# Kernel tuning notes

Measured on AMD Instinct MI355X. Metric: run time of the kernel, lower is better.

Reference implementation:

```python
import jax, jax.numpy as jnp
import numpy as np
from jax import lax

# dims
BS, C, H, W = 16, 684, 32, 128   # batch, encoder channels, feature-map H/W
Q, K, PAD = 256, 11, 5           # coverage channels, conv_Q kernel, padding
N, NP = 256, 512                 # decoder hidden n, attention dim n_prime
T = 4                            # prior attention steps stored in alpha


def setup_inputs() -> dict:
    key = jax.random.key(0)
    ks = jax.random.split(key, 10)
    s = 0.02  # small init scale (stand-in for xavier)
    return {
        "x": jax.random.normal(ks[0], (BS, C, H, W), jnp.float32),
        "st_hat": jax.random.normal(ks[1], (BS, 1, N), jnp.float32),
        "alpha": jax.random.uniform(ks[2], (BS, T, H * W), jnp.float32),
        # conv_Q: Conv2d(1, Q, k=11, pad=5)
        "convQ_w": jax.random.normal(ks[3], (Q, 1, K, K), jnp.float32) * s,
        "convQ_b": jnp.zeros((Q,), jnp.float32),
        # fc_Wa: Linear(n, n_prime)
        "Wa_w": jax.random.normal(ks[4], (NP, N), jnp.float32) * s,
        "Wa_b": jnp.zeros((NP,), jnp.float32),
        # conv_Ua: Conv2d(C, n_prime, k=1)
        "convUa_w": jax.random.normal(ks[5], (NP, C, 1, 1), jnp.float32) * s,
        "convUa_b": jnp.zeros((NP,), jnp.float32),
        # fc_Uf: Linear(Q, n_prime)
        "Uf_w": jax.random.normal(ks[6], (NP, Q), jnp.float32) * s,
        "Uf_b": jnp.zeros((NP,), jnp.float32),
        # fc_Va: Linear(n_prime, 1)
        "Va_w": jax.random.normal(ks[7], (1, NP), jnp.float32) * s,
        "Va_b": jnp.zeros((1,), jnp.float32),
    }


def reference(x, st_hat, alpha, convQ_w, convQ_b, Wa_w, Wa_b,
              convUa_w, convUa_b, Uf_w, Uf_b, Va_w, Va_b):
    bs, c, h, w = x.shape
    # beta: sum of past attention maps -> [bs, 1, h, w]
    beta = alpha.sum(axis=1).reshape(bs, 1, h, w)
    # conv_Q: coverage features [bs, Q, h, w]
    Fc = lax.conv_general_dilated(
        beta, convQ_w, window_strides=(1, 1), padding=[(PAD, PAD), (PAD, PAD)],
        dimension_numbers=("NCHW", "OIHW", "NCHW")) + convQ_b[None, :, None, None]
    # fc_Uf over channel dim after permute(2,3,0,1): [h, w, bs, n_prime]
    cover = jnp.einsum("bqhw,pq->hwbp", Fc, Uf_w) + Uf_b
    # conv_Ua (1x1 conv == per-pixel linear): [h, w, bs, n_prime]
    key = jnp.einsum("bchw,pc->hwbp", x, convUa_w[:, :, 0, 0]) + convUa_b
    # fc_Wa(st_hat).squeeze(1): [bs, n_prime]
    query = st_hat[:, 0, :] @ Wa_w.T + Wa_b
    # additive attention score
    score = jnp.tanh(key + query[None, None, :, :] + cover)  # [h,w,bs,np]
    # fc_Va -> e_t, permuted to [bs, h*w] (row-major over h,w like torch view)
    e = jnp.einsum("hwbp,p->bhw", score, Va_w[0]) + Va_b[0]
    e = e.reshape(bs, h * w)
    # softmax with the module's explicit exp/sum + eps formulation
    e_exp = jnp.exp(e)
    alpha_t = e_exp / (e_exp.sum(axis=1, keepdims=True) + 1e-8)  # [bs, hw]
    # context vector g_t = sum_n alpha_t[b,n] * x[b,c,n]
    context = jnp.einsum("bn,bcn->bc", alpha_t, x.reshape(bs, c, h * w))
    return context, alpha_t.reshape(bs, 1, h, w)
```

## Files before the change

### kernel.cpp

```cpp
#include <hip/hip_runtime.h>
#include <math.h>

#define BS 16
#define C_ 684
#define Hh 32
#define Ww 128
#define HW 4096
#define Qc 256
#define NP 512
#define Nn 256
#define NKT 26
#define NB 64

#define WS_BETA 0
#define WS_BIAS 65536
#define WS_EEXP 73728
#define WS_ESUM 139264
#define WS_ASW  139280

typedef __attribute__((ext_vector_type(8))) short bf16x8;
typedef __attribute__((ext_vector_type(4))) float f32x4;

static __device__ __forceinline__ short f2bf(float f) {
    unsigned u = __builtin_bit_cast(unsigned, f);
    u += 0x7fff + ((u >> 16) & 1);
    return (short)(u >> 16);
}

static __device__ __forceinline__ float fast_tanh(float v) {
    float ax = fabsf(v);
    float t = __expf(-2.f * ax);
    float th = (1.f - t) * __builtin_amdgcn_rcpf(1.f + t);
    return copysignf(th, v);
}

__global__ void k_prep(const float* __restrict__ alpha, const float* __restrict__ ua,
                       const float* __restrict__ ufw, const float* __restrict__ qw,
                       const float* __restrict__ st, const float* __restrict__ waw,
                       const float* __restrict__ wab, const float* __restrict__ ufb,
                       const float* __restrict__ qb, const float* __restrict__ uab,
                       float* __restrict__ beta, short* __restrict__ a_sw,
                       float* __restrict__ bias, float* __restrict__ esum) {
    int part = blockIdx.x, tid = threadIdx.x;
    if (part < 256) {
        int idx = part * 256 + tid;
        int b = idx >> 12, n = idx & 4095;
        const float* a = alpha + (size_t)b * 4 * HW + n;
        beta[idx] = a[0] + a[HW] + a[2 * HW] + a[3 * HW];
    } else if (part < 1920) {
        int idx = (part - 256) * 256 + tid;
        int j = idx & 7, m = (idx >> 3) & 511, g = (idx >> 12) & 3, kt = idx >> 14;
        int k = kt * 32 + g * 8 + j;
        float v = 0.f;
        if (k < C_) {
            v = ua[m * C_ + k];
        } else if (k < C_ + 121) {
            int tap = k - C_;
            const float* ur = ufw + m * Qc;
            float s = 0.f;
            for (int q = 0; q < Qc; ++q) s += ur[q] * qw[q * 121 + tap];
            v = s;
        }
        a_sw[idx] = f2bf(v);
    } else if (part < 1952) {
        int idx = (part - 1920) * 256 + tid;
        int b = idx >> 9, p = idx & 511;
        float s = wab[p] + ufb[p] + uab[p];
        const float* sv = st + b * Nn;
        const float* wr = waw + p * Nn;
        for (int n = 0; n < Nn; ++n) s += sv[n] * wr[n];
        const float* ur = ufw + p * Qc;
        for (int q = 0; q < Qc; ++q) s += ur[q] * qb[q];
        bias[idx] = s;
    } else {
        if (tid < BS) esum[tid] = 0.f;
    }
}

__launch_bounds__(256, 2)
__global__ void k_gemm(const short* __restrict__ a_sw, const float* __restrict__ x,
                       const float* __restrict__ beta, const float* __restrict__ bias,
                       const float* __restrict__ vaw, const float* __restrict__ vab,
                       float* __restrict__ eexp, float* __restrict__ esum) {
    __shared__ short Bs[2][4 * NB * 8];
    __shared__ float ered[4][NB];

    const int tid = threadIdx.x;
    const int lane = tid & 63, wid = tid >> 6;
    const int b = blockIdx.y, n0 = blockIdx.x * NB;
    const int q = lane >> 4, r = lane & 15;

    const int sn = tid & 63;
    const int sg = tid >> 6;
    const int n_glob = n0 + sn;
    const int pr = n_glob >> 7, pc = n_glob & 127;
    const float* xb = x + (size_t)b * C_ * HW + n_glob;
    const float* betab = beta + b * HW;

    f32x4 acc[8][4] = {};
    float fv[2][8];

    #define LDSTAGE(KT, DST)                                                  \
    {                                                                         \
        int kbase = (KT) * 32 + sg * 8;                                       \
        _Pragma("unroll")                                                     \
        for (int j = 0; j < 8; ++j) {                                         \
            int k = kbase + j;                                                \
            float f = 0.f;                                                    \
            if (k < C_) {                                                     \
                f = xb[(size_t)k * HW];                                       \
            } else if (k < C_ + 121) {                                        \
                int tap = k - C_;                                             \
                int di = tap / 11, dj = tap - di * 11;                        \
                int rr = pr + di - 5, cc = pc + dj - 5;                       \
                if (rr >= 0 && rr < Hh && cc >= 0 && cc < Ww)                 \
                    f = betab[rr * 128 + cc];                                 \
            }                                                                 \
            (DST)[j] = f;                                                     \
        }                                                                     \
    }

    LDSTAGE(0, fv[0]);
    LDSTAGE(1, fv[1]);

    const short* ap = a_sw + (size_t)(q * NP + wid * 128 + r) * 8;

    #pragma unroll 2
    for (int kt = 0; kt < NKT; ++kt) {
        bf16x8 af[8];
        const short* ak = ap + (size_t)kt * 4 * NP * 8;
        #pragma unroll
        for (int ms = 0; ms < 8; ++ms)
            af[ms] = *(const bf16x8*)(ak + ms * 16 * 8);

        {
            const float* f = fv[kt & 1];
            unsigned pk[4];
            #pragma unroll
            for (int h = 0; h < 4; ++h)
                pk[h] = (unsigned)(unsigned short)f2bf(f[2 * h]) |
                        ((unsigned)(unsigned short)f2bf(f[2 * h + 1]) << 16);
            *(uint4*)&Bs[kt & 1][(sg * NB + sn) * 8] = make_uint4(pk[0], pk[1], pk[2], pk[3]);
        }
        __syncthreads();

        bf16x8 bf[4];
        #pragma unroll
        for (int ns = 0; ns < 4; ++ns)
            bf[ns] = *(const bf16x8*)&Bs[kt & 1][(q * NB + ns * 16 + r) * 8];

        if (kt < NKT - 2) LDSTAGE(kt + 2, fv[kt & 1]);

        #pragma unroll
        for (int ms = 0; ms < 8; ++ms)
            #pragma unroll
            for (int ns = 0; ns < 4; ++ns)
                acc[ms][ns] = __builtin_amdgcn_mfma_f32_16x16x32_bf16(af[ms], bf[ns], acc[ms][ns], 0, 0, 0);
    }
    #undef LDSTAGE

    float es[4] = {0.f, 0.f, 0.f, 0.f};
    #pragma unroll
    for (int ms = 0; ms < 8; ++ms) {
        #pragma unroll
        for (int reg = 0; reg < 4; ++reg) {
            int row = wid * 128 + ms * 16 + q * 4 + reg;
            float bv = bias[b * NP + row];
            float vv = vaw[row];
            #pragma unroll
            for (int ns = 0; ns < 4; ++ns)
                es[ns] += vv * fast_tanh(acc[ms][ns][reg] + bv);
        }
    }
    #pragma unroll
    for (int ns = 0; ns < 4; ++ns) {
        es[ns] += __shfl_xor(es[ns], 16, 64);
        es[ns] += __shfl_xor(es[ns], 32, 64);
    }
    if (lane < 16) {
        #pragma unroll
        for (int ns = 0; ns < 4; ++ns) ered[wid][ns * 16 + r] = es[ns];
    }
    __syncthreads();
    if (tid < NB) {
        float s = ered[0][tid] + ered[1][tid] + ered[2][tid] + ered[3][tid] + vab[0];
        float ex = expf(s);
        eexp[b * HW + n0 + tid] = ex;
        float ps = ex;
        #pragma unroll
        for (int off = 32; off > 0; off >>= 1) ps += __shfl_xor(ps, off, 64);
        if (tid == 0) atomicAdd(&esum[b], ps);
    }
}

__global__ void k_finish(const float* __restrict__ x, const float* __restrict__ eexp,
                         const float* __restrict__ esum, float* __restrict__ ctx,
                         float* __restrict__ aout) {
    int part = blockIdx.x, b = blockIdx.y, tid = threadIdx.x;
    float iv = 1.f / (esum[b] + 1e-8f);
    if (part == 171) {
        for (int k = tid; k < HW; k += 256) aout[b * HW + k] = eexp[b * HW + k] * iv;
        return;
    }
    int wid = tid >> 6, lane = tid & 63;
    int c = part * 4 + wid;
    const float4* xr = (const float4*)(x + ((size_t)b * C_ + c) * HW);
    const float4* er = (const float4*)(eexp + b * HW);
    float acc = 0.f;
    #pragma unroll 8
    for (int k = lane; k < 1024; k += 64) {
        float4 xv = xr[k], ev = er[k];
        acc += xv.x * ev.x + xv.y * ev.y + xv.z * ev.z + xv.w * ev.w;
    }
    #pragma unroll
    for (int off = 32; off > 0; off >>= 1) acc += __shfl_xor(acc, off, 64);
    if (lane == 0) ctx[b * C_ + c] = acc * iv;
}

extern "C" void kernel_launch(void* const* d_in, const int* in_sizes, int n_in,
                              void* d_out, int out_size, void* d_ws, size_t ws_size,
                              hipStream_t stream) {
    const float* x      = (const float*)d_in[0];
    const float* st     = (const float*)d_in[1];
    const float* alpha  = (const float*)d_in[2];
    const float* convQw = (const float*)d_in[3];
    const float* convQb = (const float*)d_in[4];
    const float* Waw    = (const float*)d_in[5];
    const float* Wab    = (const float*)d_in[6];
    const float* Uaw    = (const float*)d_in[7];
    const float* Uab    = (const float*)d_in[8];
    const float* Ufw    = (const float*)d_in[9];
    const float* Ufb    = (const float*)d_in[10];
    const float* Vaw    = (const float*)d_in[11];
    const float* Vab    = (const float*)d_in[12];

    float* ws   = (float*)d_ws;
    float* beta = ws + WS_BETA;
    float* bias = ws + WS_BIAS;
    float* eexp = ws + WS_EEXP;
    float* esum = ws + WS_ESUM;
    short* a_sw = (short*)(ws + WS_ASW);

    float* ctx  = (float*)d_out;
    float* aout = (float*)d_out + BS * C_;

    k_prep<<<1953, 256, 0, stream>>>(alpha, Uaw, Ufw, convQw, st, Waw, Wab, Ufb,
                                     convQb, Uab, beta, a_sw, bias, esum);
    k_gemm<<<dim3(HW / NB, BS), 256, 0, stream>>>(a_sw, x, beta, bias, Vaw, Vab, eexp, esum);
    k_finish<<<dim3(172, BS), 256, 0, stream>>>(x, eexp, esum, ctx, aout);
}
```

Baseline: 366.8 us.

## Split attention GEMM across M halves with atomic score accumulation and separate softmax pass

Splits the 512-row attention dimension across two blocks per pixel tile, halving accumulators and raising the occupancy target. Partial scores are accumulated by atomics into a zeroed buffer. A new small kernel then computes exp and the per-batch normalizer. Each half re-streams the x/beta operand, doubling global reads and bf16 conversion work, and the change adds one launch.

```diff
diff --git a/kernel.cpp b/kernel.cpp
--- a/kernel.cpp
+++ b/kernel.cpp
@@ -15,8 +15,9 @@
 #define WS_BETA 0
 #define WS_BIAS 65536
 #define WS_EEXP 73728
-#define WS_ESUM 139264
-#define WS_ASW  139280
+#define WS_E    139264
+#define WS_INV  204800
+#define WS_ASW  204816
 
 typedef __attribute__((ext_vector_type(8))) short bf16x8;
 typedef __attribute__((ext_vector_type(4))) float f32x4;
@@ -40,7 +41,7 @@
                        const float* __restrict__ wab, const float* __restrict__ ufb,
                        const float* __restrict__ qb, const float* __restrict__ uab,
                        float* __restrict__ beta, short* __restrict__ a_sw,
-                       float* __restrict__ bias, float* __restrict__ esum) {
+                       float* __restrict__ bias, float* __restrict__ e) {
     int part = blockIdx.x, tid = threadIdx.x;
     if (part < 256) {
         int idx = part * 256 + tid;
@@ -73,22 +74,23 @@
         for (int q = 0; q < Qc; ++q) s += ur[q] * qb[q];
         bias[idx] = s;
     } else {
-        if (tid < BS) esum[tid] = 0.f;
-    }
-}
-
-__launch_bounds__(256, 2)
+        e[(part - 1952) * 256 + tid] = 0.f;
+    }
+}
+
+__launch_bounds__(256, 3)
 __global__ void k_gemm(const short* __restrict__ a_sw, const float* __restrict__ x,
                        const float* __restrict__ beta, const float* __restrict__ bias,
                        const float* __restrict__ vaw, const float* __restrict__ vab,
-                       float* __restrict__ eexp, float* __restrict__ esum) {
+                       float* __restrict__ e) {
     __shared__ short Bs[2][4 * NB * 8];
     __shared__ float ered[4][NB];
 
     const int tid = threadIdx.x;
     const int lane = tid & 63, wid = tid >> 6;
-    const int b = blockIdx.y, n0 = blockIdx.x * NB;
+    const int b = blockIdx.z, my = blockIdx.y, n0 = blockIdx.x * NB;
     const int q = lane >> 4, r = lane & 15;
+    const int m0 = my * 256;
 
     const int sn = tid & 63;
     const int sg = tid >> 6;
@@ -97,7 +99,7 @@
     const float* xb = x + (size_t)b * C_ * HW + n_glob;
     const float* betab = beta + b * HW;
 
-    f32x4 acc[8][4] = {};
+    f32x4 acc[4][4] = {};
     float fv[2][8];
 
     #define LDSTAGE(KT, DST)                                                  \
@@ -123,14 +125,14 @@
     LDSTAGE(0, fv[0]);
     LDSTAGE(1, fv[1]);
 
-    const short* ap = a_sw + (size_t)(q * NP + wid * 128 + r) * 8;
+    const short* ap = a_sw + (size_t)(q * NP + m0 + wid * 64 + r) * 8;
 
     #pragma unroll 2
     for (int kt = 0; kt < NKT; ++kt) {
-        bf16x8 af[8];
+        bf16x8 af[4];
         const short* ak = ap + (size_t)kt * 4 * NP * 8;
         #pragma unroll
-        for (int ms = 0; ms < 8; ++ms)
+        for (int ms = 0; ms < 4; ++ms)
             af[ms] = *(const bf16x8*)(ak + ms * 16 * 8);
 
         {
@@ -152,7 +154,7 @@
         if (kt < NKT - 2) LDSTAGE(kt + 2, fv[kt & 1]);
 
         #pragma unroll
-        for (int ms = 0; ms < 8; ++ms)
+        for (int ms = 0; ms < 4; ++ms)
             #pragma unroll
             for (int ns = 0; ns < 4; ++ns)
                 acc[ms][ns] = __builtin_amdgcn_mfma_f32_16x16x32_bf16(af[ms], bf[ns], acc[ms][ns], 0, 0, 0);
@@ -161,10 +163,10 @@
 
     float es[4] = {0.f, 0.f, 0.f, 0.f};
     #pragma unroll
-    for (int ms = 0; ms < 8; ++ms) {
+    for (int ms = 0; ms < 4; ++ms) {
         #pragma unroll
         for (int reg = 0; reg < 4; ++reg) {
-            int row = wid * 128 + ms * 16 + q * 4 + reg;
+            int row = m0 + wid * 64 + ms * 16 + q * 4 + reg;
             float bv = bias[b * NP + row];
             float vv = vaw[row];
             #pragma unroll
@@ -183,21 +185,39 @@
     }
     __syncthreads();
     if (tid < NB) {
-        float s = ered[0][tid] + ered[1][tid] + ered[2][tid] + ered[3][tid] + vab[0];
-        float ex = expf(s);
-        eexp[b * HW + n0 + tid] = ex;
-        float ps = ex;
-        #pragma unroll
-        for (int off = 32; off > 0; off >>= 1) ps += __shfl_xor(ps, off, 64);
-        if (tid == 0) atomicAdd(&esum[b], ps);
-    }
+        float s = ered[0][tid] + ered[1][tid] + ered[2][tid] + ered[3][tid];
+        if (my == 0) s += vab[0];
+        atomicAdd(&e[b * HW + n0 + tid], s);
+    }
+}
+
+__global__ void k_mid(const float* __restrict__ e, float* __restrict__ eexp,
+                      float* __restrict__ inv) {
+    __shared__ float sred[256];
+    int b = blockIdx.x, tid = threadIdx.x;
+    float vloc[16];
+    float ps = 0.f;
+#pragma unroll
+    for (int k = 0; k < 16; ++k) {
+        vloc[k] = expf(e[b * HW + tid + k * 256]);
+        ps += vloc[k];
+    }
+#pragma unroll
+    for (int k = 0; k < 16; ++k) eexp[b * HW + tid + k * 256] = vloc[k];
+    sred[tid] = ps;
+    __syncthreads();
+    for (int s = 128; s > 0; s >>= 1) {
+        if (tid < s) sred[tid] += sred[tid + s];
+        __syncthreads();
+    }
+    if (tid == 0) inv[b] = 1.f / (sred[0] + 1e-8f);
 }
 
 __global__ void k_finish(const float* __restrict__ x, const float* __restrict__ eexp,
-                         const float* __restrict__ esum, float* __restrict__ ctx,
+                         const float* __restrict__ inv, float* __restrict__ ctx,
                          float* __restrict__ aout) {
     int part = blockIdx.x, b = blockIdx.y, tid = threadIdx.x;
-    float iv = 1.f / (esum[b] + 1e-8f);
+    float iv = inv[b];
     if (part == 171) {
         for (int k = tid; k < HW; k += 256) aout[b * HW + k] = eexp[b * HW + k] * iv;
         return;
@@ -238,14 +258,16 @@
     float* beta = ws + WS_BETA;
     float* bias = ws + WS_BIAS;
     float* eexp = ws + WS_EEXP;
-    float* esum = ws + WS_ESUM;
+    float* e    = ws + WS_E;
+    float* inv  = ws + WS_INV;
     short* a_sw = (short*)(ws + WS_ASW);
 
     float* ctx  = (float*)d_out;
     float* aout = (float*)d_out + BS * C_;
 
-    k_prep<<<1953, 256, 0, stream>>>(alpha, Uaw, Ufw, convQw, st, Waw, Wab, Ufb,
-                                     convQb, Uab, beta, a_sw, bias, esum);
-    k_gemm<<<dim3(HW / NB, BS), 256, 0, stream>>>(a_sw, x, beta, bias, Vaw, Vab, eexp, esum);
-    k_finish<<<dim3(172, BS), 256, 0, stream>>>(x, eexp, esum, ctx, aout);
-}
+    k_prep<<<2208, 256, 0, stream>>>(alpha, Uaw, Ufw, convQw, st, Waw, Wab, Ufb,
+                                     convQb, Uab, beta, a_sw, bias, e);
+    k_gemm<<<dim3(HW / NB, 2, BS), 256, 0, stream>>>(a_sw, x, beta, bias, Vaw, Vab, e);
+    k_mid<<<BS, 256, 0, stream>>>(e, eexp, inv);
+    k_finish<<<dim3(172, BS), 256, 0, stream>>>(x, eexp, inv, ctx, aout);
+}
```

Result: slower. 374.2 us (+2.0%).
